# Kernel tuning notes

Hardware: AMD Instinct MI355X
Metric: run time of the kernel (lower is better)

Reference implementation:

```python
import jax, jax.numpy as jnp
import numpy as np

EMBED = 1024
HEAD = 128

def setup_inputs() -> dict:
    key = jax.random.key(0)
    k1, k2, k3, k4 = jax.random.split(key, 4)
    x = jax.random.normal(k1, (4, 4096, EMBED), dtype=jnp.float32)
    # nn.Linear default init ~ U(-1/sqrt(fan_in), 1/sqrt(fan_in)); weights stored as [in, out] for x @ W
    s = 1.0 / np.sqrt(EMBED)
    Wq = jax.random.uniform(k2, (EMBED, HEAD), dtype=jnp.float32, minval=-s, maxval=s)
    Wk = jax.random.uniform(k3, (EMBED, HEAD), dtype=jnp.float32, minval=-s, maxval=s)
    Wv = jax.random.uniform(k4, (EMBED, HEAD), dtype=jnp.float32, minval=-s, maxval=s)
    return {"x": x, "Wq": Wq, "Wk": Wk, "Wv": Wv}

def reference(x, Wq, Wk, Wv):
    # x: [B, S, E]
    B, S, E = x.shape
    q = x @ Wq  # [B, S, H]
    k = x @ Wk
    v = x @ Wv
    scale = jnp.asarray(k.shape[-1], x.dtype) ** -0.5
    scores = jnp.einsum('bqh,bkh->bqk', q, k) * scale  # [B, S, S]
    causal = jnp.tril(jnp.ones((S, S), dtype=bool))
    scores = jnp.where(causal, scores, jnp.asarray(-jnp.inf, x.dtype))
    attn = jax.nn.softmax(scores, axis=-1)
    return jnp.einsum('bqk,bkh->bqh', attn, v)  # [B, S, H]
```

## Files before the change

### kernel.cpp

```cpp
#include <hip/hip_runtime.h>
#include <math.h>

#define BATCH 4
#define SEQ   4096
#define EMB   1024
#define HD    128
#define MROWS (BATCH*SEQ)
#define SCALE  0.08838834764831844f
#define SCALEQ 0.12751742f
#define CHUNK 10
#define NJOBS 119
#define MAXC  7

typedef __attribute__((ext_vector_type(8))) short bf16x8;
typedef __attribute__((ext_vector_type(4))) short short4v;
typedef __attribute__((ext_vector_type(4))) float f32x4;
typedef __attribute__((ext_vector_type(4))) int   i32x4;

static __device__ __forceinline__ unsigned short f2bf(float f) {
    unsigned int u = __float_as_uint(f);
    u += 0x7fff + ((u >> 16) & 1);
    return (unsigned short)(u >> 16);
}
static __device__ __forceinline__ float bf2f(unsigned short s) {
    return __uint_as_float((unsigned int)s << 16);
}
static __device__ __forceinline__ short4v pack4(float4 a) {
    short4v p;
    p[0] = (short)f2bf(a.x); p[1] = (short)f2bf(a.y);
    p[2] = (short)f2bf(a.z); p[3] = (short)f2bf(a.w);
    return p;
}

__global__ __launch_bounds__(256) void wtrans_kernel(
    const float* __restrict__ Wq, const float* __restrict__ Wk,
    const float* __restrict__ Wv, unsigned short* __restrict__ Wt)
{
    __shared__ __align__(16) unsigned short Xs[16 * 132];
    const int w  = blockIdx.y;
    const float* W = (w == 0) ? Wq : (w == 1) ? Wk : Wv;
    const float sc = (w == 0) ? SCALEQ : 1.0f;
    unsigned short* dst = Wt + (size_t)w * 131072;
    const int k0 = blockIdx.x * 16;
    const int t  = threadIdx.x;

#pragma unroll
    for (int i = 0; i < 2; ++i) {
        int gg = i * 256 + t;
        int row = gg >> 5, c4 = gg & 31;
        float4 a = *(const float4*)&W[(size_t)(k0 + row) * HD + c4 * 4];
        short4v p;
        p[0] = (short)f2bf(a.x * sc); p[1] = (short)f2bf(a.y * sc);
        p[2] = (short)f2bf(a.z * sc); p[3] = (short)f2bf(a.w * sc);
        *(short4v*)&Xs[row * 132 + c4 * 4] = p;
    }
    __syncthreads();
    const int n = t >> 1, half = t & 1;
    i32x4 o;
#pragma unroll
    for (int e = 0; e < 4; ++e) {
        unsigned int lo = Xs[(half * 8 + e * 2    ) * 132 + n];
        unsigned int hi = Xs[(half * 8 + e * 2 + 1) * 132 + n];
        o[e] = (int)(lo | (hi << 16));
    }
    *(i32x4*)&dst[(size_t)n * 1024 + k0 + half * 8] = o;
}

__global__ __launch_bounds__(512, 4) void qkv_kernel(
    const float* __restrict__ x, const unsigned short* __restrict__ Wt,
    unsigned short* __restrict__ qb, unsigned short* __restrict__ kb,
    unsigned short* __restrict__ vtb)
{
    __shared__ __align__(16) unsigned short lds[13824];
    unsigned short* xs0 = lds;
    unsigned short* xs1 = lds + 2304;

    const int t    = threadIdx.x;
    const int lane = t & 63, ng = t >> 6;
    const int quad = lane >> 4, l16 = lane & 15;
    const int m0   = blockIdx.x * 32;

    f32x4 acc[2][3];
#pragma unroll
    for (int i = 0; i < 2; ++i)
#pragma unroll
        for (int j = 0; j < 3; ++j) acc[i][j] = (f32x4){0.f, 0.f, 0.f, 0.f};

    const int xrow = t >> 4, xseg = t & 15;
    const float* xbase = x + (size_t)(m0 + xrow) * EMB + xseg * 4;
    const unsigned short* Wb = Wt + ((size_t)(ng * 48 + l16)) * 1024 + quad * 8;

    bf16x8 aB0[2][3], aB1[2][3];
    float4 xr;

    {
        float4 a = *(const float4*)&xbase[0];
#pragma unroll
        for (int ks = 0; ks < 2; ++ks)
#pragma unroll
            for (int jt = 0; jt < 3; ++jt)
                aB0[ks][jt] = *(const bf16x8*)&Wb[(size_t)jt * 16384 + ks * 32];
        *(short4v*)&xs0[xrow * 72 + xseg * 4] = pack4(a);
        xr = *(const float4*)&xbase[64];
    }
    asm volatile("s_waitcnt lgkmcnt(0)" ::: "memory");
    __builtin_amdgcn_s_barrier();

    for (int kt = 0; kt < EMB; kt += 128) {
        *(short4v*)&xs1[xrow * 72 + xseg * 4] = pack4(xr);
        if (kt + 128 < EMB)
            xr = *(const float4*)&xbase[kt + 128];
#pragma unroll
        for (int ks = 0; ks < 2; ++ks)
#pragma unroll
            for (int jt = 0; jt < 3; ++jt)
                aB1[ks][jt] = *(const bf16x8*)&Wb[(size_t)jt * 16384 + kt + 64 + ks * 32];
        {
            bf16x8 aA[2][2];
#pragma unroll
            for (int ks = 0; ks < 2; ++ks)
#pragma unroll
                for (int mt = 0; mt < 2; ++mt)
                    aA[ks][mt] = *(const bf16x8*)&xs0[(mt * 16 + l16) * 72 + ks * 32 + quad * 8];
            __builtin_amdgcn_s_setprio(1);
#pragma unroll
            for (int ks = 0; ks < 2; ++ks)
#pragma unroll
                for (int mt = 0; mt < 2; ++mt)
#pragma unroll
                    for (int jt = 0; jt < 3; ++jt)
                        acc[mt][jt] = __builtin_amdgcn_mfma_f32_16x16x32_bf16(
                            aA[ks][mt], aB0[ks][jt], acc[mt][jt], 0, 0, 0);
            __builtin_amdgcn_s_setprio(0);
        }
        asm volatile("s_waitcnt lgkmcnt(0)" ::: "memory");
        __builtin_amdgcn_s_barrier();

        if (kt + 128 < EMB) {
            *(short4v*)&xs0[xrow * 72 + xseg * 4] = pack4(xr);
            if (kt + 192 < EMB)
                xr = *(const float4*)&xbase[kt + 192];
#pragma unroll
            for (int ks = 0; ks < 2; ++ks)
#pragma unroll
                for (int jt = 0; jt < 3; ++jt)
                    aB0[ks][jt] = *(const bf16x8*)&Wb[(size_t)jt * 16384 + kt + 128 + ks * 32];
        }
        {
            bf16x8 aA[2][2];
#pragma unroll
            for (int ks = 0; ks < 2; ++ks)
#pragma unroll
                for (int mt = 0; mt < 2; ++mt)
                    aA[ks][mt] = *(const bf16x8*)&xs1[(mt * 16 + l16) * 72 + ks * 32 + quad * 8];
            __builtin_amdgcn_s_setprio(1);
#pragma unroll
            for (int ks = 0; ks < 2; ++ks)
#pragma unroll
                for (int mt = 0; mt < 2; ++mt)
#pragma unroll
                    for (int jt = 0; jt < 3; ++jt)
                        acc[mt][jt] = __builtin_amdgcn_mfma_f32_16x16x32_bf16(
                            aA[ks][mt], aB1[ks][jt], acc[mt][jt], 0, 0, 0);
            __builtin_amdgcn_s_setprio(0);
        }
        asm volatile("s_waitcnt lgkmcnt(0)" ::: "memory");
        __builtin_amdgcn_s_barrier();
    }

    unsigned short* Cq = lds;
    unsigned short* Ck = lds + 32 * 136;
    unsigned short* Cv = lds + 2 * 32 * 136;
#pragma unroll
    for (int mt = 0; mt < 2; ++mt)
#pragma unroll
        for (int jt = 0; jt < 3; ++jt) {
            int nt = ng * 3 + jt;
            int wm = nt >> 3, nl = nt & 7;
            if (wm < 2) {
                unsigned short* C = (wm == 0) ? Cq : Ck;
#pragma unroll
                for (int rr = 0; rr < 4; ++rr)
                    C[(mt * 16 + quad * 4 + rr) * 136 + nl * 16 + l16] =
                        f2bf(acc[mt][jt][rr]);
            } else {
                short4v p;
                p[0] = (short)f2bf(acc[mt][jt][0]); p[1] = (short)f2bf(acc[mt][jt][1]);
                p[2] = (short)f2bf(acc[mt][jt][2]); p[3] = (short)f2bf(acc[mt][jt][3]);
                *(short4v*)&Cv[(nl * 16 + l16) * 40 + mt * 16 + quad * 4] = p;
            }
        }
    __syncthreads();
    {
        int row = t >> 4, seg = t & 15;
        *(i32x4*)&qb[((size_t)(m0 + row)) * HD + seg * 8] = *(const i32x4*)&Cq[row * 136 + seg * 8];
        *(i32x4*)&kb[((size_t)(m0 + row)) * HD + seg * 8] = *(const i32x4*)&Ck[row * 136 + seg * 8];
    }
    {
        const int b = m0 >> 12, s0 = m0 & 4095;
        int h = t >> 2, seg = t & 3;
        *(i32x4*)&vtb[(size_t)b * (HD * SEQ) + (size_t)h * SEQ + s0 + seg * 8] =
            *(const i32x4*)&Cv[h * 40 + seg * 8];
    }
}

#define PADK 136
#define PADV 72
#define PADP 72
#define DEFER_THR 8.0f

__global__ __launch_bounds__(512, 4) void flash_kernel(
    const unsigned short* __restrict__ qb, const unsigned short* __restrict__ kb,
    const unsigned short* __restrict__ vtb, unsigned short* __restrict__ Opart,
    float* __restrict__ mbuf, float* __restrict__ lbuf)
{
    __shared__ __align__(16) unsigned short Ks[64 * PADK];
    __shared__ __align__(16) unsigned short Vt[128 * PADV];
    __shared__ __align__(16) unsigned short Pt[128 * PADP];

    const int bx   = blockIdx.x;
    const int slot = bx & 7, pp = bx >> 3;
    const int b    = slot >> 1;
    const int jj   = pp * 2 + (slot & 1);
    if (jj >= NJOBS) return;

    const int t    = threadIdx.x;
    const int lane = t & 63, w = t >> 6;
    const int quad = lane >> 4, l16 = lane & 15;

    int qi = 0, s = 0;
    for (qi = 0; qi < 32; ++qi) {
        int cnt = (qi + 5) / 5;
        if (jj < s + cnt) break;
        s += cnt;
    }
    const int c    = jj - s;
    const int qrow = qi * 128 + w * 16 + l16;
    const int jmax = 2 * qi + 2;
    const int jbeg = c * CHUNK;
    const int jend = min(jbeg + CHUNK, jmax);
    const int wtop = qi * 128 + w * 16;

    bf16x8 qf[4];
    {
        const unsigned short* qp = qb + ((size_t)b * SEQ + qrow) * HD;
#pragma unroll
        for (int ks = 0; ks < 4; ++ks)
            qf[ks] = *(const bf16x8*)&qp[ks * 32 + quad * 8];
    }

    f32x4 O[8];
#pragma unroll
    for (int i = 0; i < 8; ++i) O[i] = (f32x4){0.f, 0.f, 0.f, 0.f};
    float m_run = -1e30f, l_run = 0.f;

    const unsigned short* kbb  = kb  + (size_t)b * SEQ * HD;
    const unsigned short* vtbb = vtb + (size_t)b * HD * SEQ;

    const int gg0 = t, gg1 = 512 + t;
    i32x4 kr0, kr1, vr0, vr1;
    kr0 = *(const i32x4*)&kbb[(size_t)jbeg * 64 * HD + (size_t)gg0 * 8];
    kr1 = *(const i32x4*)&kbb[(size_t)jbeg * 64 * HD + (size_t)gg1 * 8];
    vr0 = *(const i32x4*)&vtbb[(size_t)(gg0 >> 3) * SEQ + jbeg * 64 + (gg0 & 7) * 8];
    vr1 = *(const i32x4*)&vtbb[(size_t)(gg1 >> 3) * SEQ + jbeg * 64 + (gg1 & 7) * 8];

    for (int j0 = jbeg; j0 < jend; ++j0) {
        __syncthreads();
        *(i32x4*)&Ks[(gg0 >> 4) * PADK + (gg0 & 15) * 8] = kr0;
        *(i32x4*)&Ks[(gg1 >> 4) * PADK + (gg1 & 15) * 8] = kr1;
        *(i32x4*)&Vt[(gg0 >> 3) * PADV + (gg0 & 7) * 8] = vr0;
        *(i32x4*)&Vt[(gg1 >> 3) * PADV + (gg1 & 7) * 8] = vr1;
        __syncthreads();

        if (j0 + 1 < jend) {
            const int j1 = j0 + 1;
            kr0 = *(const i32x4*)&kbb[(size_t)j1 * 64 * HD + (size_t)gg0 * 8];
            kr1 = *(const i32x4*)&kbb[(size_t)j1 * 64 * HD + (size_t)gg1 * 8];
            vr0 = *(const i32x4*)&vtbb[(size_t)(gg0 >> 3) * SEQ + j1 * 64 + (gg0 & 7) * 8];
            vr1 = *(const i32x4*)&vtbb[(size_t)(gg1 >> 3) * SEQ + j1 * 64 + (gg1 & 7) * 8];
        }

        if (j0 * 64 > wtop + 15) continue;

        f32x4 st[4];
        __builtin_amdgcn_s_setprio(1);
#pragma unroll
        for (int mt = 0; mt < 4; ++mt) {
            f32x4 a = (f32x4){0.f, 0.f, 0.f, 0.f};
#pragma unroll
            for (int ks = 0; ks < 4; ++ks) {
                bf16x8 kf = *(const bf16x8*)&Ks[(mt * 16 + l16) * PADK + ks * 32 + quad * 8];
                a = __builtin_amdgcn_mfma_f32_16x16x32_bf16(kf, qf[ks], a, 0, 0, 0);
            }
            st[mt] = a;
        }
        __builtin_amdgcn_s_setprio(0);

        if (j0 * 64 + 63 > wtop) {
#pragma unroll
            for (int mt = 0; mt < 4; ++mt)
#pragma unroll
                for (int rr = 0; rr < 4; ++rr) {
                    int kv = j0 * 64 + mt * 16 + quad * 4 + rr;
                    if (kv > qrow) st[mt][rr] = -1e30f;
                }
        }

        float mx = -1e30f;
#pragma unroll
        for (int mt = 0; mt < 4; ++mt)
#pragma unroll
            for (int rr = 0; rr < 4; ++rr) mx = fmaxf(mx, st[mt][rr]);
        mx = fmaxf(mx, __shfl_xor(mx, 16));
        mx = fmaxf(mx, __shfl_xor(mx, 32));
        if (!__all(mx <= m_run + DEFER_THR)) {
            const float m_new = fmaxf(m_run, mx);
            const float alpha = exp2f(m_run - m_new);
            l_run *= alpha;
#pragma unroll
            for (int i = 0; i < 8; ++i) {
                O[i][0] *= alpha; O[i][1] *= alpha; O[i][2] *= alpha; O[i][3] *= alpha;
            }
            m_run = m_new;
        }
        float psum = 0.f;
#pragma unroll
        for (int mt = 0; mt < 4; ++mt)
#pragma unroll
            for (int rr = 0; rr < 4; ++rr) {
                float p = exp2f(st[mt][rr] - m_run);
                st[mt][rr] = p;
                psum += p;
            }
        psum += __shfl_xor(psum, 16);
        psum += __shfl_xor(psum, 32);
        l_run += psum;

#pragma unroll
        for (int mt = 0; mt < 4; ++mt) {
            short4v p;
            p[0] = (short)f2bf(st[mt][0]); p[1] = (short)f2bf(st[mt][1]);
            p[2] = (short)f2bf(st[mt][2]); p[3] = (short)f2bf(st[mt][3]);
            *(short4v*)&Pt[(w * 16 + l16) * PADP + mt * 16 + quad * 4] = p;
        }

        bf16x8 pf0 = *(const bf16x8*)&Pt[(w * 16 + l16) * PADP + quad * 8];
        bf16x8 pf1 = *(const bf16x8*)&Pt[(w * 16 + l16) * PADP + 32 + quad * 8];
        __builtin_amdgcn_s_setprio(1);
#pragma unroll
        for (int mt = 0; mt < 8; ++mt) {
            bf16x8 vf0 = *(const bf16x8*)&Vt[(mt * 16 + l16) * PADV + quad * 8];
            bf16x8 vf1 = *(const bf16x8*)&Vt[(mt * 16 + l16) * PADV + 32 + quad * 8];
            O[mt] = __builtin_amdgcn_mfma_f32_16x16x32_bf16(vf0, pf0, O[mt], 0, 0, 0);
            O[mt] = __builtin_amdgcn_mfma_f32_16x16x32_bf16(vf1, pf1, O[mt], 0, 0, 0);
        }
        __builtin_amdgcn_s_setprio(0);
    }

    const int r = w * 16 + l16;
    const size_t jobbase = (size_t)b * NJOBS + jj;
    unsigned short* po = Opart + jobbase * (128 * 128) + (size_t)r * 128;
#pragma unroll
    for (int mt = 0; mt < 8; ++mt) {
        short4v p;
        p[0] = (short)f2bf(O[mt][0]); p[1] = (short)f2bf(O[mt][1]);
        p[2] = (short)f2bf(O[mt][2]); p[3] = (short)f2bf(O[mt][3]);
        *(short4v*)&po[mt * 16 + quad * 4] = p;
    }
    if (quad == 0) {
        mbuf[jobbase * 128 + r] = m_run;
        lbuf[jobbase * 128 + r] = l_run;
    }
}

__global__ __launch_bounds__(512) void combine_kernel(
    const unsigned short* __restrict__ Opart, const float* __restrict__ mbuf,
    const float* __restrict__ lbuf, float* __restrict__ out)
{
    const int qi = blockIdx.x, b = blockIdx.y;
    const int nc = (qi + 5) / 5;
    int j0 = 0;
    for (int q = 0; q < qi; ++q) j0 += (q + 5) / 5;
    const int t = threadIdx.x;
    const int row = t >> 2, cg = (t & 3) * 32;

    float mv[MAXC], lv[MAXC];
    float M = -1e30f;
#pragma unroll
    for (int c2 = 0; c2 < MAXC; ++c2) {
        if (c2 < nc) {
            const size_t jb = (size_t)b * NJOBS + j0 + c2;
            mv[c2] = mbuf[jb * 128 + row];
            lv[c2] = lbuf[jb * 128 + row];
            M = fmaxf(M, mv[c2]);
        } else { mv[c2] = -1e30f; lv[c2] = 0.f; }
    }
    float L = 0.f;
#pragma unroll
    for (int c2 = 0; c2 < MAXC; ++c2)
        if (c2 < nc) L += exp2f(mv[c2] - M) * lv[c2];
    const float Linv = 1.0f / L;

    float acc[32];
#pragma unroll
    for (int i = 0; i < 32; ++i) acc[i] = 0.f;
#pragma unroll
    for (int c2 = 0; c2 < MAXC; ++c2) {
        if (c2 < nc) {
            const float wgt = exp2f(mv[c2] - M) * Linv;
            const unsigned short* po = Opart + ((size_t)b * NJOBS + j0 + c2) * (128 * 128) +
                                       (size_t)row * 128 + cg;
#pragma unroll
            for (int i = 0; i < 4; ++i) {
                i32x4 d = *(const i32x4*)&po[i * 8];
#pragma unroll
                for (int e = 0; e < 4; ++e) {
                    unsigned int u = (unsigned int)d[e];
                    acc[i * 8 + e * 2]     = fmaf(wgt, bf2f((unsigned short)(u & 0xffff)), acc[i * 8 + e * 2]);
                    acc[i * 8 + e * 2 + 1] = fmaf(wgt, bf2f((unsigned short)(u >> 16)),   acc[i * 8 + e * 2 + 1]);
                }
            }
        }
    }
    float* op = out + ((size_t)b * SEQ + qi * 128 + row) * HD + cg;
#pragma unroll
    for (int i = 0; i < 8; ++i) {
        float4 res;
        res.x = acc[i * 4]; res.y = acc[i * 4 + 1];
        res.z = acc[i * 4 + 2]; res.w = acc[i * 4 + 3];
        *(float4*)&op[i * 4] = res;
    }
}

extern "C" void kernel_launch(void* const* d_in, const int* in_sizes, int n_in,
                              void* d_out, int out_size, void* d_ws, size_t ws_size,
                              hipStream_t stream) {
    const float* x  = (const float*)d_in[0];
    const float* Wq = (const float*)d_in[1];
    const float* Wk = (const float*)d_in[2];
    const float* Wv = (const float*)d_in[3];

    unsigned short* qb    = (unsigned short*)d_ws;
    unsigned short* kb    = qb  + (size_t)MROWS * HD;
    unsigned short* vtb   = kb  + (size_t)MROWS * HD;
    unsigned short* Wt    = vtb + (size_t)MROWS * HD;
    unsigned short* Opart = Wt  + (size_t)3 * HD * EMB;
    float* mbuf = (float*)(Opart + (size_t)BATCH * NJOBS * 128 * 128);
    float* lbuf = mbuf + (size_t)BATCH * NJOBS * 128;
    float* out = (float*)d_out;

    wtrans_kernel <<<dim3(64, 3),  dim3(256), 0, stream>>>(Wq, Wk, Wv, Wt);
    qkv_kernel    <<<dim3(512),    dim3(512), 0, stream>>>(x, Wt, qb, kb, vtb);
    flash_kernel  <<<dim3(480),    dim3(512), 0, stream>>>(qb, kb, vtb, Opart, mbuf, lbuf);
    combine_kernel<<<dim3(32, 4),  dim3(512), 0, stream>>>(Opart, mbuf, lbuf, out);
}
```

Baseline: 187.8 us.

## Double QKV projection M-tile and pre-swizzle weights into MFMA fragment layout

The QKV projection kernel now processes 64 rows per block instead of 32, halving the grid and doubling weight-fragment reuse per block. The weight transpose kernel writes W directly in per-lane MFMA fragment order, so each wave's B-operand load becomes a contiguous 1KB read instead of strided row reads. The cost is more accumulator registers and LDS per block, with the occupancy bound dropped to 2 waves' worth, and only 256 blocks to fill the GPU.

After: 171.5 us. 8.7% less time.

```diff
diff --git a/kernel.cpp b/kernel.cpp
--- a/kernel.cpp
+++ b/kernel.cpp
@@ -40,8 +40,8 @@
     const int w  = blockIdx.y;
     const float* W = (w == 0) ? Wq : (w == 1) ? Wk : Wv;
     const float sc = (w == 0) ? SCALEQ : 1.0f;
-    unsigned short* dst = Wt + (size_t)w * 131072;
-    const int k0 = blockIdx.x * 16;
+    const int bx = blockIdx.x;
+    const int k0 = bx * 16;
     const int t  = threadIdx.x;
 
 #pragma unroll
@@ -55,78 +55,97 @@
         *(short4v*)&Xs[row * 132 + c4 * 4] = p;
     }
     __syncthreads();
-    const int n = t >> 1, half = t & 1;
+    const int n = t >> 1, g = t & 1;
     i32x4 o;
 #pragma unroll
     for (int e = 0; e < 4; ++e) {
-        unsigned int lo = Xs[(half * 8 + e * 2    ) * 132 + n];
-        unsigned int hi = Xs[(half * 8 + e * 2 + 1) * 132 + n];
+        unsigned int lo = Xs[(g * 8 + e * 2    ) * 132 + n];
+        unsigned int hi = Xs[(g * 8 + e * 2 + 1) * 132 + n];
         o[e] = (int)(lo | (hi << 16));
     }
-    *(i32x4*)&dst[(size_t)n * 1024 + k0 + half * 8] = o;
-}
-
-__global__ __launch_bounds__(512, 4) void qkv_kernel(
+    const int ntg  = w * 8 + (n >> 4);
+    const int kc   = bx >> 1;
+    const int quad = (bx * 2 + g) & 3;
+    const int lane = quad * 16 + (n & 15);
+    *(i32x4*)&Wt[(((size_t)ntg * 32 + kc) * 64 + lane) * 8] = o;
+}
+
+__global__ __launch_bounds__(512, 2) void qkv_kernel(
     const float* __restrict__ x, const unsigned short* __restrict__ Wt,
     unsigned short* __restrict__ qb, unsigned short* __restrict__ kb,
     unsigned short* __restrict__ vtb)
 {
-    __shared__ __align__(16) unsigned short lds[13824];
+    __shared__ __align__(16) unsigned short lds[26624];
     unsigned short* xs0 = lds;
-    unsigned short* xs1 = lds + 2304;
+    unsigned short* xs1 = lds + 4608;
 
     const int t    = threadIdx.x;
     const int lane = t & 63, ng = t >> 6;
     const int quad = lane >> 4, l16 = lane & 15;
-    const int m0   = blockIdx.x * 32;
-
-    f32x4 acc[2][3];
-#pragma unroll
-    for (int i = 0; i < 2; ++i)
+    const int m0   = blockIdx.x * 64;
+
+    f32x4 acc[4][3];
+#pragma unroll
+    for (int i = 0; i < 4; ++i)
 #pragma unroll
         for (int j = 0; j < 3; ++j) acc[i][j] = (f32x4){0.f, 0.f, 0.f, 0.f};
 
-    const int xrow = t >> 4, xseg = t & 15;
-    const float* xbase = x + (size_t)(m0 + xrow) * EMB + xseg * 4;
-    const unsigned short* Wb = Wt + ((size_t)(ng * 48 + l16)) * 1024 + quad * 8;
+    const int xr0 = t >> 4,        xs0c = (t & 15) * 4;
+    const int xr1 = (t + 512) >> 4, xs1c = ((t + 512) & 15) * 4;
+    const float* xb0 = x + (size_t)(m0 + xr0) * EMB + xs0c;
+    const float* xb1 = x + (size_t)(m0 + xr1) * EMB + xs1c;
+
+    const unsigned short* Wl = Wt + (size_t)lane * 8;
+    const size_t jb0 = (size_t)(ng * 3 + 0) * 16384;
+    const size_t jb1 = (size_t)(ng * 3 + 1) * 16384;
+    const size_t jb2 = (size_t)(ng * 3 + 2) * 16384;
 
     bf16x8 aB0[2][3], aB1[2][3];
-    float4 xr;
+    float4 xra, xrb;
 
     {
-        float4 a = *(const float4*)&xbase[0];
-#pragma unroll
-        for (int ks = 0; ks < 2; ++ks)
-#pragma unroll
-            for (int jt = 0; jt < 3; ++jt)
-                aB0[ks][jt] = *(const bf16x8*)&Wb[(size_t)jt * 16384 + ks * 32];
-        *(short4v*)&xs0[xrow * 72 + xseg * 4] = pack4(a);
-        xr = *(const float4*)&xbase[64];
+        float4 a = *(const float4*)&xb0[0];
+        float4 b = *(const float4*)&xb1[0];
+#pragma unroll
+        for (int ks = 0; ks < 2; ++ks) {
+            aB0[ks][0] = *(const bf16x8*)&Wl[jb0 + (size_t)ks * 512];
+            aB0[ks][1] = *(const bf16x8*)&Wl[jb1 + (size_t)ks * 512];
+            aB0[ks][2] = *(const bf16x8*)&Wl[jb2 + (size_t)ks * 512];
+        }
+        *(short4v*)&xs0[xr0 * 72 + xs0c] = pack4(a);
+        *(short4v*)&xs0[xr1 * 72 + xs1c] = pack4(b);
+        xra = *(const float4*)&xb0[64];
+        xrb = *(const float4*)&xb1[64];
     }
     asm volatile("s_waitcnt lgkmcnt(0)" ::: "memory");
     __builtin_amdgcn_s_barrier();
 
     for (int kt = 0; kt < EMB; kt += 128) {
-        *(short4v*)&xs1[xrow * 72 + xseg * 4] = pack4(xr);
-        if (kt + 128 < EMB)
-            xr = *(const float4*)&xbase[kt + 128];
-#pragma unroll
-        for (int ks = 0; ks < 2; ++ks)
-#pragma unroll
-            for (int jt = 0; jt < 3; ++jt)
-                aB1[ks][jt] = *(const bf16x8*)&Wb[(size_t)jt * 16384 + kt + 64 + ks * 32];
+        const size_t kcA = (size_t)(kt >> 5);
+        *(short4v*)&xs1[xr0 * 72 + xs0c] = pack4(xra);
+        *(short4v*)&xs1[xr1 * 72 + xs1c] = pack4(xrb);
+        if (kt + 128 < EMB) {
+            xra = *(const float4*)&xb0[kt + 128];
+            xrb = *(const float4*)&xb1[kt + 128];
+        }
+#pragma unroll
+        for (int ks = 0; ks < 2; ++ks) {
+            aB1[ks][0] = *(const bf16x8*)&Wl[jb0 + (kcA + 2 + ks) * 512];
+            aB1[ks][1] = *(const bf16x8*)&Wl[jb1 + (kcA + 2 + ks) * 512];
+            aB1[ks][2] = *(const bf16x8*)&Wl[jb2 + (kcA + 2 + ks) * 512];
+        }
         {
-            bf16x8 aA[2][2];
+            bf16x8 aA[2][4];
 #pragma unroll
             for (int ks = 0; ks < 2; ++ks)
 #pragma unroll
-                for (int mt = 0; mt < 2; ++mt)
+                for (int mt = 0; mt < 4; ++mt)
                     aA[ks][mt] = *(const bf16x8*)&xs0[(mt * 16 + l16) * 72 + ks * 32 + quad * 8];
             __builtin_amdgcn_s_setprio(1);
 #pragma unroll
             for (int ks = 0; ks < 2; ++ks)
 #pragma unroll
-                for (int mt = 0; mt < 2; ++mt)
+                for (int mt = 0; mt < 4; ++mt)
 #pragma unroll
                     for (int jt = 0; jt < 3; ++jt)
                         acc[mt][jt] = __builtin_amdgcn_mfma_f32_16x16x32_bf16(
@@ -137,27 +156,31 @@
         __builtin_amdgcn_s_barrier();
 
         if (kt + 128 < EMB) {
-            *(short4v*)&xs0[xrow * 72 + xseg * 4] = pack4(xr);
-            if (kt + 192 < EMB)
-                xr = *(const float4*)&xbase[kt + 192];
+            *(short4v*)&xs0[xr0 * 72 + xs0c] = pack4(xra);
+            *(short4v*)&xs0[xr1 * 72 + xs1c] = pack4(xrb);
+            if (kt + 192 < EMB) {
+                xra = *(const float4*)&xb0[kt + 192];
+                xrb = *(const float4*)&xb1[kt + 192];
+            }
+#pragma unroll
+            for (int ks = 0; ks < 2; ++ks) {
+                aB0[ks][0] = *(const bf16x8*)&Wl[jb0 + (kcA + 4 + ks) * 512];
+                aB0[ks][1] = *(const bf16x8*)&Wl[jb1 + (kcA + 4 + ks) * 512];
+                aB0[ks][2] = *(const bf16x8*)&Wl[jb2 + (kcA + 4 + ks) * 512];
+            }
+        }
+        {
+            bf16x8 aA[2][4];
 #pragma unroll
             for (int ks = 0; ks < 2; ++ks)
 #pragma unroll
-                for (int jt = 0; jt < 3; ++jt)
-                    aB0[ks][jt] = *(const bf16x8*)&Wb[(size_t)jt * 16384 + kt + 128 + ks * 32];
-        }
-        {
-            bf16x8 aA[2][2];
-#pragma unroll
-            for (int ks = 0; ks < 2; ++ks)
-#pragma unroll
-                for (int mt = 0; mt < 2; ++mt)
+                for (int mt = 0; mt < 4; ++mt)
                     aA[ks][mt] = *(const bf16x8*)&xs1[(mt * 16 + l16) * 72 + ks * 32 + quad * 8];
             __builtin_amdgcn_s_setprio(1);
 #pragma unroll
             for (int ks = 0; ks < 2; ++ks)
 #pragma unroll
-                for (int mt = 0; mt < 2; ++mt)
+                for (int mt = 0; mt < 4; ++mt)
 #pragma unroll
                     for (int jt = 0; jt < 3; ++jt)
                         acc[mt][jt] = __builtin_amdgcn_mfma_f32_16x16x32_bf16(
@@ -169,10 +192,10 @@
     }
 
     unsigned short* Cq = lds;
-    unsigned short* Ck = lds + 32 * 136;
-    unsigned short* Cv = lds + 2 * 32 * 136;
-#pragma unroll
-    for (int mt = 0; mt < 2; ++mt)
+    unsigned short* Ck = lds + 64 * 136;
+    unsigned short* Cv = lds + 2 * 64 * 136;
+#pragma unroll
+    for (int mt = 0; mt < 4; ++mt)
 #pragma unroll
         for (int jt = 0; jt < 3; ++jt) {
             int nt = ng * 3 + jt;
@@ -187,20 +210,28 @@
                 short4v p;
                 p[0] = (short)f2bf(acc[mt][jt][0]); p[1] = (short)f2bf(acc[mt][jt][1]);
                 p[2] = (short)f2bf(acc[mt][jt][2]); p[3] = (short)f2bf(acc[mt][jt][3]);
-                *(short4v*)&Cv[(nl * 16 + l16) * 40 + mt * 16 + quad * 4] = p;
+                *(short4v*)&Cv[(nl * 16 + l16) * 72 + mt * 16 + quad * 4] = p;
             }
         }
     __syncthreads();
     {
-        int row = t >> 4, seg = t & 15;
-        *(i32x4*)&qb[((size_t)(m0 + row)) * HD + seg * 8] = *(const i32x4*)&Cq[row * 136 + seg * 8];
-        *(i32x4*)&kb[((size_t)(m0 + row)) * HD + seg * 8] = *(const i32x4*)&Ck[row * 136 + seg * 8];
+#pragma unroll
+        for (int i = 0; i < 2; ++i) {
+            int idx = i * 512 + t;
+            int row = idx >> 4, seg = idx & 15;
+            *(i32x4*)&qb[((size_t)(m0 + row)) * HD + seg * 8] = *(const i32x4*)&Cq[row * 136 + seg * 8];
+            *(i32x4*)&kb[((size_t)(m0 + row)) * HD + seg * 8] = *(const i32x4*)&Ck[row * 136 + seg * 8];
+        }
     }
     {
         const int b = m0 >> 12, s0 = m0 & 4095;
-        int h = t >> 2, seg = t & 3;
-        *(i32x4*)&vtb[(size_t)b * (HD * SEQ) + (size_t)h * SEQ + s0 + seg * 8] =
-            *(const i32x4*)&Cv[h * 40 + seg * 8];
+#pragma unroll
+        for (int i = 0; i < 2; ++i) {
+            int idx = i * 512 + t;
+            int h = idx >> 3, seg = idx & 7;
+            *(i32x4*)&vtb[(size_t)b * (HD * SEQ) + (size_t)h * SEQ + s0 + seg * 8] =
+                *(const i32x4*)&Cv[h * 72 + seg * 8];
+        }
     }
 }
 
@@ -450,7 +481,7 @@
     float* out = (float*)d_out;
 
     wtrans_kernel <<<dim3(64, 3),  dim3(256), 0, stream>>>(Wq, Wk, Wv, Wt);
-    qkv_kernel    <<<dim3(512),    dim3(512), 0, stream>>>(x, Wt, qb, kb, vtb);
+    qkv_kernel    <<<dim3(256),    dim3(512), 0, stream>>>(x, Wt, qb, kb, vtb);
     flash_kernel  <<<dim3(480),    dim3(512), 0, stream>>>(qb, kb, vtb, Opart, mbuf, lbuf);
     combine_kernel<<<dim3(32, 4),  dim3(512), 0, stream>>>(Opart, mbuf, lbuf, out);
 }
```
